# Optimization experiments

Hardware: AMD Instinct MI355X
Metric: run time of the kernel (lower is better)

Reference implementation:

```python
import jax, jax.numpy as jnp
import numpy as np

D_MODEL = 1024
D_STATE = 64
HEADDIM = 64
D_INNER = 2 * D_MODEL          # expand=2 -> 2048
NHEADS = D_INNER // HEADDIM    # 32
D_IN_PROJ = 2 * D_INNER + 2 * D_STATE + NHEADS  # 4256 (ngroups=1)
CHANNELS = D_INNER + 2 * D_STATE                # 2176
KSIZE = 4
LN_EPS = 1e-5


def setup_inputs() -> dict:
    key = jax.random.key(0)
    ks = jax.random.split(key, 8)
    B, L = 2, 2048
    u = jax.random.normal(ks[0], (B, L, D_MODEL), jnp.float32)
    W_in1 = jax.random.normal(ks[1], (D_IN_PROJ, D_MODEL), jnp.float32) * 0.02
    A_log = jnp.log(jax.random.uniform(ks[2], (NHEADS,), jnp.float32, 1.0, 16.0))
    conv_w = jax.random.normal(ks[3], (CHANNELS, CHANNELS, KSIZE), jnp.float32) / np.sqrt(CHANNELS * KSIZE)
    conv_b = jax.random.normal(ks[4], (CHANNELS,), jnp.float32) * 0.01
    prelu_a = jnp.array(0.25, jnp.float32)
    W_in2 = jax.random.normal(ks[5], (D_INNER, D_MODEL), jnp.float32) * 0.02
    W_in3 = jax.random.normal(ks[6], (D_MODEL, D_INNER), jnp.float32) * 0.02
    ln_g = jnp.ones((D_INNER,), jnp.float32)
    ln_b = jnp.zeros((D_INNER,), jnp.float32)
    return {"u": u, "W_in1": W_in1, "A_log": A_log, "conv_w": conv_w, "conv_b": conv_b,
            "prelu_a": prelu_a, "W_in2": W_in2, "W_in3": W_in3, "ln_g": ln_g, "ln_b": ln_b}


def _segsum(x):
    # x: (..., T) -> (..., T, T), lower-triangular segment sums, -inf above diag
    T = x.shape[-1]
    cs = jnp.cumsum(x, axis=-1)
    seg = cs[..., :, None] - cs[..., None, :]
    mask = jnp.tril(jnp.ones((T, T), bool))
    return jnp.where(mask, seg, -jnp.inf)


def _ssd(X, A, B, C, block_len):
    # X:(b,L,h,p)  A:(b,L,h)  B,C:(b,L,n)  (ngroups=1, group axis squeezed)
    b, Lseq, h, p = X.shape
    c = Lseq // block_len
    X = X.reshape(b, c, block_len, h, p)
    A = A.reshape(b, c, block_len, h).transpose(0, 3, 1, 2)      # (b,h,c,l)
    B = B.reshape(b, c, block_len, -1)                            # (b,c,l,n)
    C = C.reshape(b, c, block_len, -1)
    A_cumsum = jnp.cumsum(A, axis=-1)                             # (b,h,c,l)
    Lmat = jnp.exp(_segsum(A))                                    # (b,h,c,l,l)
    Y_diag = jnp.einsum('bcln,bcsn,bhcls,bcshp->bclhp', C, B, Lmat, X)
    decay_states = jnp.exp(A_cumsum[..., -1:] - A_cumsum)         # (b,h,c,l)
    states = jnp.einsum('bcln,bhcl,bclhp->bchpn', B, decay_states, X)
    init = jnp.zeros_like(states[:, :1])
    states = jnp.concatenate([init, states], axis=1)              # (b,c+1,h,p,n)
    A_last = jnp.pad(A_cumsum[..., -1], ((0, 0), (0, 0), (1, 0)))
    decay_chunk = jnp.exp(_segsum(A_last))                        # (b,h,c+1,c+1)
    new_states = jnp.einsum('bhzc,bchpn->bzhpn', decay_chunk, states)
    states_off, final_state = new_states[:, :-1], new_states[:, -1]
    state_decay_out = jnp.exp(A_cumsum)
    Y_off = jnp.einsum('bcln,bchpn,bhcl->bclhp', C, states_off, state_decay_out)
    Y = (Y_diag + Y_off).reshape(b, Lseq, h, p)
    return Y, final_state


def reference(u, W_in1, A_log, conv_w, conv_b, prelu_a, W_in2, W_in3, ln_g, ln_b):
    Bsz, L, _ = u.shape
    zxbcdt = u @ W_in1.T                                          # (B,L,4256); d_nonssm=0
    A = -jnp.exp(A_log)
    z = zxbcdt[..., :D_INNER]                                     # split but unused (as in source)
    xBC = zxbcdt[..., D_INNER:D_INNER + CHANNELS]
    dt = zxbcdt[..., D_INNER + CHANNELS:]
    dt_safe = jnp.where(dt <= 20.0, dt, 0.0)
    dt = jnp.where(dt <= 20.0, jnp.log1p(jnp.exp(dt_safe)), dt)   # softplus w/ overflow guard
    A_t = dt * A[None, None, :]                                   # (B,L,H)
    # causal conv (left-pad k-1) + PReLU
    xt = xBC.transpose(0, 2, 1)                                   # (B,C,L)
    conv = jax.lax.conv_general_dilated(xt, conv_w, (1,), [(KSIZE - 1, 0)],
                                        dimension_numbers=('NCH', 'OIH', 'NCH'))
    conv = conv + conv_b[None, :, None]
    conv = jnp.maximum(conv, 0) + prelu_a * jnp.minimum(conv, 0)
    xBC_conv = conv.transpose(0, 2, 1)                            # (B,L,C)
    x = xBC_conv[..., :D_INNER].reshape(Bsz, L, NHEADS, HEADDIM)
    Bmat = xBC_conv[..., D_INNER:D_INNER + D_STATE]
    Cmat = xBC_conv[..., D_INNER + D_STATE:]
    Y, _ = _ssd(x, A_t, Bmat, Cmat, L // 4)
    out = Y.reshape(Bsz, L, D_INNER)
    u2 = jax.nn.gelu(u @ W_in2.T, approximate=False)
    h = u2 * out
    mu = jnp.mean(h, axis=-1, keepdims=True)
    var = jnp.mean((h - mu) ** 2, axis=-1, keepdims=True)
    hn = (h - mu) / jnp.sqrt(var + LN_EPS) * ln_g + ln_b
    return hn @ W_in3.T
```

## Files before the change

kernel.cpp:

```cpp
#include <hip/hip_runtime.h>
#include <stdint.h>

typedef unsigned short u16;
typedef _Float16 f16x8 __attribute__((ext_vector_type(8)));
typedef float f32x4 __attribute__((ext_vector_type(4)));

#define AS1C const __attribute__((address_space(1))) void*
#define AS3P __attribute__((address_space(3))) void*

#define DM 1024
#define DI 2048
#define CHN 2176
#define ROWS 4096
#define PADR_U 2051

__device__ __forceinline__ float h2f(u16 v) {
    union { u16 u; _Float16 h; } x; x.u = v; return (float)x.h;
}
__device__ __forceinline__ u16 f2h(float f) {
    union { _Float16 h; u16 u; } x; x.h = (_Float16)f; return x.u;
}

template<int EPI, int TERMS>
__global__ __launch_bounds__(256) void split_gemm(
    const u16* __restrict__ Ah, const u16* __restrict__ Al,
    const u16* __restrict__ Bh,
    float* __restrict__ Cf, u16* __restrict__ Oh,
    int K, int ldA, int ldB, int ldC)
{
    __shared__ u16 Ash[128 * 64];
    __shared__ u16 Asl[TERMS == 2 ? 128 * 64 : 64];
    __shared__ u16 Bsh[128 * 64];
    const int tid = threadIdx.x;
    const int bm = blockIdx.x * 128;
    const int bn = blockIdx.y * 128;
    const int lane = tid & 63;
    const int w = tid >> 6, wr = w >> 1, wc = w & 1;
    const int lrow = lane & 15;
    const int cb = lane >> 4;
    const int trow = tid >> 3;
    const int tcolS = (((tid & 7) ^ (trow & 7)) << 3);

    f32x4 acc[4][4];
#pragma unroll
    for (int m = 0; m < 4; ++m)
#pragma unroll
        for (int n = 0; n < 4; ++n) acc[m][n] = f32x4{0.f, 0.f, 0.f, 0.f};

    for (int k0 = 0; k0 < K; k0 += 64) {
#pragma unroll
        for (int ch = 0; ch < 4; ++ch) {
            int r = bm + ch * 32 + trow;
            long aoff = (long)r * ldA + k0 + tcolS;
            __builtin_amdgcn_global_load_lds((AS1C)(Ah + aoff), (AS3P)(&Ash[ch * 2048 + tid * 8]), 16, 0, 0);
            if constexpr (TERMS == 2)
                __builtin_amdgcn_global_load_lds((AS1C)(Al + aoff), (AS3P)(&Asl[ch * 2048 + tid * 8]), 16, 0, 0);
            int rr = bn + ch * 32 + trow;
            long boff = (long)rr * ldB + k0 + tcolS;
            __builtin_amdgcn_global_load_lds((AS1C)(Bh + boff), (AS3P)(&Bsh[ch * 2048 + tid * 8]), 16, 0, 0);
        }
        __syncthreads();
#pragma unroll
        for (int kk = 0; kk < 64; kk += 32) {
            const int swz = ((((kk >> 3) + cb) ^ (lrow & 7)) << 3);
            f16x8 ah[4], al[4], bh[4];
#pragma unroll
            for (int m = 0; m < 4; ++m) {
                int o = (wr * 64 + m * 16 + lrow) * 64 + swz;
                ah[m] = *(const f16x8*)&Ash[o];
                if constexpr (TERMS == 2) al[m] = *(const f16x8*)&Asl[o];
            }
#pragma unroll
            for (int n = 0; n < 4; ++n)
                bh[n] = *(const f16x8*)&Bsh[(wc * 64 + n * 16 + lrow) * 64 + swz];
#pragma unroll
            for (int m = 0; m < 4; ++m)
#pragma unroll
                for (int n = 0; n < 4; ++n) {
                    acc[m][n] = __builtin_amdgcn_mfma_f32_16x16x32_f16(ah[m], bh[n], acc[m][n], 0, 0, 0);
                    if constexpr (TERMS == 2)
                        acc[m][n] = __builtin_amdgcn_mfma_f32_16x16x32_f16(al[m], bh[n], acc[m][n], 0, 0, 0);
                }
        }
        __syncthreads();
    }

#pragma unroll
    for (int m = 0; m < 4; ++m) {
#pragma unroll
        for (int n = 0; n < 4; ++n) {
            int col = bn + wc * 64 + n * 16 + lrow;
            int rbase = bm + wr * 64 + m * 16 + ((lane >> 4) << 2);
#pragma unroll
            for (int j = 0; j < 4; ++j) {
                int r = rbase + j;
                float v = acc[m][n][j];
                if (EPI == 0) {
                    Cf[(long)r * ldC + col] = v;
                } else {
                    int kc = r / CHN;
                    int o = r - kc * CHN;
                    Oh[(long)o * 4096 + kc * 1024 + col] = f2h(v);
                }
            }
        }
    }
}

__global__ __launch_bounds__(256) void conv_g2(
    const u16* __restrict__ up, const u16* __restrict__ Wbig, const u16* __restrict__ W2,
    float* __restrict__ Xf, float* __restrict__ Bm, float* __restrict__ Cm,
    float* __restrict__ u2raw,
    const float* __restrict__ bias, const float* __restrict__ prelu)
{
    __shared__ u16 Ash[128 * 64];
    __shared__ u16 Bsh[128 * 64];
    const int tid = threadIdx.x;
    const bool isconv = blockIdx.y < 17;
    const u16* __restrict__ Bmat = isconv ? Wbig : W2;
    const int K = isconv ? 4096 : 1024;
    const int ldB = K;
    const int aoffR = isconv ? 0 : 3;
    const int bm = blockIdx.x * 128;
    const int bn = (isconv ? blockIdx.y : blockIdx.y - 17) * 128;
    const int lane = tid & 63;
    const int w = tid >> 6, wr = w >> 1, wc = w & 1;
    const int lrow = lane & 15;
    const int cb = lane >> 4;
    const int trow = tid >> 3;
    const int tcolS = (((tid & 7) ^ (trow & 7)) << 3);

    f32x4 acc[4][4];
#pragma unroll
    for (int m = 0; m < 4; ++m)
#pragma unroll
        for (int n = 0; n < 4; ++n) acc[m][n] = f32x4{0.f, 0.f, 0.f, 0.f};

    for (int k0 = 0; k0 < K; k0 += 64) {
        const int kc = k0 >> 10;
        const int i0 = k0 & 1023;
#pragma unroll
        for (int ch = 0; ch < 4; ++ch) {
            int r = bm + ch * 32 + trow;
            long srow = (long)(r >> 11) * PADR_U + (r & 2047) + kc + aoffR;
            long aoff = srow * 1024 + i0 + tcolS;
            __builtin_amdgcn_global_load_lds((AS1C)(up + aoff), (AS3P)(&Ash[ch * 2048 + tid * 8]), 16, 0, 0);
            int rr = bn + ch * 32 + trow;
            long boff = (long)rr * ldB + k0 + tcolS;
            __builtin_amdgcn_global_load_lds((AS1C)(Bmat + boff), (AS3P)(&Bsh[ch * 2048 + tid * 8]), 16, 0, 0);
        }
        __syncthreads();
#pragma unroll
        for (int kk = 0; kk < 64; kk += 32) {
            const int swz = ((((kk >> 3) + cb) ^ (lrow & 7)) << 3);
            f16x8 a[4], b[4];
#pragma unroll
            for (int m = 0; m < 4; ++m)
                a[m] = *(const f16x8*)&Ash[(wr * 64 + m * 16 + lrow) * 64 + swz];
#pragma unroll
            for (int n = 0; n < 4; ++n)
                b[n] = *(const f16x8*)&Bsh[(wc * 64 + n * 16 + lrow) * 64 + swz];
#pragma unroll
            for (int m = 0; m < 4; ++m)
#pragma unroll
                for (int n = 0; n < 4; ++n)
                    acc[m][n] = __builtin_amdgcn_mfma_f32_16x16x32_f16(a[m], b[n], acc[m][n], 0, 0, 0);
        }
        __syncthreads();
    }

    const float pa = isconv ? *prelu : 0.f;
#pragma unroll
    for (int m = 0; m < 4; ++m) {
#pragma unroll
        for (int n = 0; n < 4; ++n) {
            int col = bn + wc * 64 + n * 16 + lrow;
            int rbase = bm + wr * 64 + m * 16 + ((lane >> 4) << 2);
            float bv = isconv ? bias[col] : 0.f;
#pragma unroll
            for (int j = 0; j < 4; ++j) {
                int r = rbase + j;
                float v = acc[m][n][j];
                if (isconv) {
                    v += bv;
                    v = v > 0.f ? v : pa * v;
                    if (col < DI) Xf[(long)r * DI + col] = v;
                    else if (col < DI + 64) Bm[r * 64 + (col - DI)] = v;
                    else Cm[r * 64 + (col - DI - 64)] = v;
                } else {
                    u2raw[(long)r * 2048 + col] = v;
                }
            }
        }
    }
}

__global__ void conv_w_h(const float* __restrict__ w, u16* __restrict__ ch_) {
    int idx = blockIdx.x * 256 + threadIdx.x;
    if (idx < CHN * CHN) {
        int o = idx / CHN, i = idx - o * CHN;
        f32x4 v = *(const f32x4*)&w[(long)idx * 4];
#pragma unroll
        for (int kc = 0; kc < 4; ++kc)
            ch_[(long)(kc * CHN + o) * CHN + i] = f2h(v[kc]);
    }
}

__global__ __launch_bounds__(256) void w1x_t(
    const float* __restrict__ W1, u16* __restrict__ th)
{
    __shared__ float tile[32][33];
    int i0 = blockIdx.x * 32, d0 = blockIdx.y * 32;
    int ti = threadIdx.x & 31, tj = threadIdx.x >> 5;
#pragma unroll
    for (int rr = 0; rr < 32; rr += 8)
        tile[tj + rr][ti] = W1[(long)(2048 + i0 + tj + rr) * 1024 + d0 + ti];
    __syncthreads();
#pragma unroll
    for (int rr = 0; rr < 32; rr += 8)
        th[(long)(d0 + tj + rr) * CHN + i0 + ti] = f2h(tile[ti][tj + rr]);
}

__global__ void u_pad_f16(const float* __restrict__ u, u16* __restrict__ ph) {
    int idx = blockIdx.x * 256 + threadIdx.x;
    if (idx >= 2 * PADR_U * 256) return;
    int row = idx >> 8, c4 = (idx & 255) << 2;
    int b = row >= PADR_U ? 1 : 0;
    int lr = row - b * PADR_U;
    ushort4 h = {0, 0, 0, 0};
    if (lr >= 3) {
        f32x4 v = *(const f32x4*)&u[((long)(b * 2048 + lr - 3)) * 1024 + c4];
        h.x = f2h(v[0]); h.y = f2h(v[1]); h.z = f2h(v[2]); h.w = f2h(v[3]);
    }
    *(ushort4*)&ph[(long)idx * 4] = h;
}

__global__ void cast_f16(const float* __restrict__ in, u16* __restrict__ oh, int n4) {
    int idx = blockIdx.x * 256 + threadIdx.x;
    if (idx < n4) {
        f32x4 v = *(const f32x4*)&in[(long)idx * 4];
        ushort4 h;
        h.x = f2h(v[0]); h.y = f2h(v[1]); h.z = f2h(v[2]); h.w = f2h(v[3]);
        *(ushort4*)&oh[(long)idx * 4] = h;
    }
}

__global__ __launch_bounds__(256) void dt_kernel(
    const float* __restrict__ u, const float* __restrict__ W1,
    const float* __restrict__ A_log, float* __restrict__ A_t)
{
    __shared__ float us[8][1024];
    int r0 = blockIdx.x * 8;
    int tid = threadIdx.x;
#pragma unroll
    for (int rep = 0; rep < 8; ++rep) {
        int idx = rep * 256 + tid;
        int i = idx >> 8, kx = (idx & 255) << 2;
        *(f32x4*)&us[i][kx] = *(const f32x4*)&u[(long)(r0 + i) * 1024 + kx];
    }
    __syncthreads();
    int row = tid >> 5;
    int hh = tid & 31;
    const float* wrow = W1 + (long)(4224 + hh) * 1024;
    f32x4 a4 = {0.f, 0.f, 0.f, 0.f};
#pragma unroll 4
    for (int k = 0; k < 1024; k += 4) {
        f32x4 a = *(const f32x4*)&us[row][k];
        f32x4 b = *(const f32x4*)&wrow[k];
        a4 += a * b;
    }
    float dt = a4[0] + a4[1] + a4[2] + a4[3];
    if (dt <= 20.f) dt = log1pf(__expf(dt));
    float At = dt * (-__expf(A_log[hh]));
    int r = r0 + row;
    int b = r >> 11, l = r & 2047;
    A_t[((long)(b * 32 + hh)) * 2048 + l] = At;
}

__global__ __launch_bounds__(64) void csum_chunk(float* A_t, float* __restrict__ Atot)
{
    int bid = blockIdx.x;
    int lane = threadIdx.x;
    float* p = A_t + (long)bid * 128;
    float v0 = p[lane * 2], v1 = p[lane * 2 + 1];
    float s = v0 + v1;
    float t = s;
#pragma unroll
    for (int d = 1; d < 64; d <<= 1) {
        float o = __shfl_up(t, d);
        if (lane >= d) t += o;
    }
    float excl = t - s;
    p[lane * 2] = excl + v0;
    p[lane * 2 + 1] = excl + s;
    if (lane == 63) Atot[bid] = t;
}

__global__ __launch_bounds__(256) void g_chunk(
    const float* __restrict__ Cm, const float* __restrict__ Bm, float* __restrict__ G)
{
    __shared__ float CsT[128 * 33];
    __shared__ float BsT[128 * 33];
    const int bid = blockIdx.x;
    const int b = bid >> 4, c = bid & 15;
    const long rowbase = (long)b * 2048 + c * 128;
    const int tid = threadIdx.x;
    const int li = tid & 15, si = tid >> 4;
    const int l0 = li * 8, s0 = si * 8;
    float acc[8][8];
#pragma unroll
    for (int i = 0; i < 8; ++i)
#pragma unroll
        for (int j = 0; j < 8; ++j) acc[i][j] = 0.f;

    for (int kt = 0; kt < 2; ++kt) {
        __syncthreads();
#pragma unroll
        for (int t = 0; t < 16; ++t) {
            int idx = t * 256 + tid;
            int row = idx >> 5, k = idx & 31;
            CsT[row * 33 + k] = Cm[(rowbase + row) * 64 + kt * 32 + k];
            BsT[row * 33 + k] = Bm[(rowbase + row) * 64 + kt * 32 + k];
        }
        __syncthreads();
        for (int k = 0; k < 32; ++k) {
            float cv[8], bv[8];
#pragma unroll
            for (int i = 0; i < 8; ++i) cv[i] = CsT[(l0 + i) * 33 + k];
#pragma unroll
            for (int j = 0; j < 8; ++j) bv[j] = BsT[(s0 + j) * 33 + k];
#pragma unroll
            for (int i = 0; i < 8; ++i)
#pragma unroll
                for (int j = 0; j < 8; ++j) acc[i][j] += cv[i] * bv[j];
        }
    }
    float* gz = G + (long)bid * 16384;
#pragma unroll
    for (int i = 0; i < 8; ++i) {
        f32x4 o0 = {acc[i][0], acc[i][1], acc[i][2], acc[i][3]};
        f32x4 o1 = {acc[i][4], acc[i][5], acc[i][6], acc[i][7]};
        *(f32x4*)&gz[(l0 + i) * 128 + s0] = o0;
        *(f32x4*)&gz[(l0 + i) * 128 + s0 + 4] = o1;
    }
}

__global__ __launch_bounds__(256) void ssd_diag_states(
    float* XY, const float* __restrict__ Bm, const float* __restrict__ G,
    const float* __restrict__ cs, const float* __restrict__ Atot, float* __restrict__ Sc)
{
    __shared__ float Xs[128 * 64];
    __shared__ float Gb[32 * 132];
    __shared__ float csL[128];
    __shared__ float dsL[128];
    const int bid = blockIdx.x;
    const int bh = bid >> 4, c = bid & 15;
    const int b = bh >> 5, h = bh & 31;
    const long rowbase = (long)b * 2048 + c * 128;
    const float* gz = G + (long)(b * 16 + c) * 16384;
    const float atot = Atot[bid];
    const int tid = threadIdx.x;

    if (tid < 128) csL[tid] = cs[(long)bh * 2048 + c * 128 + tid];
#pragma unroll
    for (int t = 0; t < 8; ++t) {
        int idx = t * 256 + tid;
        int row = idx >> 4, c4 = (idx & 15) << 2;
        *(f32x4*)&Xs[row * 64 + c4] = *(const f32x4*)&XY[(rowbase + row) * 2048 + h * 64 + c4];
    }
    __syncthreads();
    if (tid < 128) dsL[tid] = __expf(atot - csL[tid]);

    const int lg = tid & 31, pg = tid >> 5;
    const int l0 = lg * 4, p0 = pg * 8;
    float cl[4];
#pragma unroll
    for (int i = 0; i < 4; ++i) cl[i] = csL[l0 + i];
    float acc1[4][8];
#pragma unroll
    for (int i = 0; i < 4; ++i)
#pragma unroll
        for (int j = 0; j < 8; ++j) acc1[i][j] = 0.f;

    for (int st = 0; st < 4; ++st) {
        __syncthreads();
#pragma unroll
        for (int t = 0; t < 16; ++t) {
            int idx = t * 256 + tid;
            int l = idx >> 5, sq = idx & 31;
            Gb[sq * 132 + l] = gz[l * 128 + st * 32 + sq];
        }
        __syncthreads();
        for (int sq = 0; sq < 32; ++sq) {
            int s = st * 32 + sq;
            float css = csL[s];
            f32x4 x0 = *(const f32x4*)&Xs[s * 64 + p0];
            f32x4 x1 = *(const f32x4*)&Xs[s * 64 + p0 + 4];
#pragma unroll
            for (int i = 0; i < 4; ++i) {
                int l = l0 + i;
                float P = (s <= l) ? Gb[sq * 132 + l] * __expf(cl[i] - css) : 0.f;
                acc1[i][0] += P * x0[0]; acc1[i][1] += P * x0[1];
                acc1[i][2] += P * x0[2]; acc1[i][3] += P * x0[3];
                acc1[i][4] += P * x1[0]; acc1[i][5] += P * x1[1];
                acc1[i][6] += P * x1[2]; acc1[i][7] += P * x1[3];
            }
        }
    }

    const int pq = tid & 15, nq = tid >> 4;
    const int pp0 = pq * 4, nn0 = nq * 4;
    float acc2[4][4];
#pragma unroll
    for (int i = 0; i < 4; ++i)
#pragma unroll
        for (int j = 0; j < 4; ++j) acc2[i][j] = 0.f;
    for (int half = 0; half < 2; ++half) {
        __syncthreads();
#pragma unroll
        for (int t = 0; t < 4; ++t) {
            int idx = t * 256 + tid;
            int srow = idx >> 4, c4 = (idx & 15) << 2;
            *(f32x4*)&Gb[srow * 64 + c4] = *(const f32x4*)&Bm[(rowbase + half * 64 + srow) * 64 + c4];
        }
        __syncthreads();
        for (int ss = 0; ss < 64; ++ss) {
            int s = half * 64 + ss;
            float d = dsL[s];
            f32x4 xv = *(const f32x4*)&Xs[s * 64 + pp0];
            f32x4 bv = *(const f32x4*)&Gb[ss * 64 + nn0];
            float xd[4];
#pragma unroll
            for (int i = 0; i < 4; ++i) xd[i] = xv[i] * d;
#pragma unroll
            for (int i = 0; i < 4; ++i)
#pragma unroll
                for (int j = 0; j < 4; ++j) acc2[i][j] += xd[i] * bv[j];
        }
    }
    long scb = (long)bid * 4096;
#pragma unroll
    for (int i = 0; i < 4; ++i) {
        f32x4 o = {acc2[i][0], acc2[i][1], acc2[i][2], acc2[i][3]};
        *(f32x4*)&Sc[scb + (pp0 + i) * 64 + nn0] = o;
    }
#pragma unroll
    for (int i = 0; i < 4; ++i) {
        f32x4 y0 = {acc1[i][0], acc1[i][1], acc1[i][2], acc1[i][3]};
        f32x4 y1 = {acc1[i][4], acc1[i][5], acc1[i][6], acc1[i][7]};
        long yo = (rowbase + l0 + i) * 2048 + h * 64 + p0;
        *(f32x4*)&XY[yo] = y0;
        *(f32x4*)&XY[yo + 4] = y1;
    }
}

__global__ __launch_bounds__(256) void ssd_combine(float* Sc, const float* __restrict__ Atot)
{
    int bh = blockIdx.x >> 2;
    int q = blockIdx.x & 3;
    int tid = threadIdx.x;
    float run[4];
#pragma unroll
    for (int t = 0; t < 4; ++t) run[t] = 0.f;
    for (int c = 0; c < 16; ++c) {
        float e = __expf(Atot[bh * 16 + c]);
        long base = (long)(bh * 16 + c) * 4096 + q * 1024;
#pragma unroll
        for (int t = 0; t < 4; ++t) {
            long idx = base + t * 256 + tid;
            float tmp = Sc[idx];
            Sc[idx] = run[t];
            run[t] = e * run[t] + tmp;
        }
    }
}

__global__ __launch_bounds__(256) void ssd_yoff(
    const float* __restrict__ Cm, const float* __restrict__ Sin,
    const float* __restrict__ cs, float* XY)
{
    __shared__ float Cs[128 * 66];
    __shared__ float St[64 * 68];
    __shared__ float csL[128];
    const int bid = blockIdx.x;
    const int bh = bid >> 4, c = bid & 15;
    const int b = bh >> 5, h = bh & 31;
    const long rowbase = (long)b * 2048 + c * 128;
    const int tid = threadIdx.x;

    if (tid < 128) csL[tid] = cs[(long)bh * 2048 + c * 128 + tid];
#pragma unroll
    for (int t = 0; t < 32; ++t) {
        int idx = t * 256 + tid;
        int row = idx >> 6, n = idx & 63;
        Cs[row * 66 + n] = Cm[(rowbase + row) * 64 + n];
    }
#pragma unroll
    for (int t = 0; t < 16; ++t) {
        int idx = t * 256 + tid;
        int p = idx >> 6, n = idx & 63;
        St[n * 68 + p] = Sin[(long)bid * 4096 + p * 64 + n];
    }
    __syncthreads();

    const int lg = tid & 31, pg = tid >> 5;
    const int l0 = lg * 4, p0 = pg * 8;
    float el[4];
#pragma unroll
    for (int i = 0; i < 4; ++i) el[i] = __expf(csL[l0 + i]);
    float acc[4][8];
#pragma unroll
    for (int i = 0; i < 4; ++i)
#pragma unroll
        for (int j = 0; j < 8; ++j) acc[i][j] = 0.f;

    for (int n = 0; n < 64; ++n) {
        float cv[4];
#pragma unroll
        for (int i = 0; i < 4; ++i) cv[i] = Cs[(l0 + i) * 66 + n];
        f32x4 s0 = *(const f32x4*)&St[n * 68 + p0];
        f32x4 s1 = *(const f32x4*)&St[n * 68 + p0 + 4];
#pragma unroll
        for (int i = 0; i < 4; ++i) {
            acc[i][0] += cv[i] * s0[0]; acc[i][1] += cv[i] * s0[1];
            acc[i][2] += cv[i] * s0[2]; acc[i][3] += cv[i] * s0[3];
            acc[i][4] += cv[i] * s1[0]; acc[i][5] += cv[i] * s1[1];
            acc[i][6] += cv[i] * s1[2]; acc[i][7] += cv[i] * s1[3];
        }
    }
#pragma unroll
    for (int i = 0; i < 4; ++i) {
        long yo = (rowbase + l0 + i) * 2048 + h * 64 + p0;
        f32x4 y0 = *(const f32x4*)&XY[yo];
        f32x4 y1 = *(const f32x4*)&XY[yo + 4];
        y0[0] += el[i] * acc[i][0]; y0[1] += el[i] * acc[i][1];
        y0[2] += el[i] * acc[i][2]; y0[3] += el[i] * acc[i][3];
        y1[0] += el[i] * acc[i][4]; y1[1] += el[i] * acc[i][5];
        y1[2] += el[i] * acc[i][6]; y1[3] += el[i] * acc[i][7];
        *(f32x4*)&XY[yo] = y0;
        *(f32x4*)&XY[yo + 4] = y1;
    }
}

__global__ __launch_bounds__(256) void ln_kernel(
    const float* __restrict__ u2raw, const float* __restrict__ Y,
    const float* __restrict__ lng, const float* __restrict__ lnb,
    u16* __restrict__ hh)
{
    __shared__ float hbuf[2048];
    __shared__ float rs[4], rs2[4];
    int r = blockIdx.x;
    int tid = threadIdx.x;
    float s = 0.f, s2 = 0.f;
    for (int j = tid; j < 2048; j += 256) {
        float x = u2raw[(long)r * 2048 + j];
        float g = 0.5f * x * (1.f + erff(x * 0.70710678118654752f));
        float hv = g * Y[(long)r * 2048 + j];
        hbuf[j] = hv;
        s += hv;
        s2 += hv * hv;
    }
    for (int d = 32; d > 0; d >>= 1) {
        s += __shfl_down(s, d);
        s2 += __shfl_down(s2, d);
    }
    if ((tid & 63) == 0) { rs[tid >> 6] = s; rs2[tid >> 6] = s2; }
    __syncthreads();
    float tot = rs[0] + rs[1] + rs[2] + rs[3];
    float tot2 = rs2[0] + rs2[1] + rs2[2] + rs2[3];
    float mu = tot * (1.f / 2048.f);
    float var = tot2 * (1.f / 2048.f) - mu * mu;
    float inv = rsqrtf(var + 1e-5f);
    for (int j = tid; j < 2048; j += 256) {
        float v = (hbuf[j] - mu) * inv * lng[j] + lnb[j];
        hh[(long)r * 2048 + j] = f2h(v);
    }
}

extern "C" void kernel_launch(void* const* d_in, const int* in_sizes, int n_in,
                              void* d_out, int out_size, void* d_ws, size_t ws_size,
                              hipStream_t stream) {
    const float* u = (const float*)d_in[0];
    const float* W1 = (const float*)d_in[1];
    const float* A_log = (const float*)d_in[2];
    const float* convw = (const float*)d_in[3];
    const float* convb = (const float*)d_in[4];
    const float* prelu = (const float*)d_in[5];
    const float* W2 = (const float*)d_in[6];
    const float* W3 = (const float*)d_in[7];
    const float* lng = (const float*)d_in[8];
    const float* lnb = (const float*)d_in[9];
    float* out = (float*)d_out;

    char* base = (char*)d_ws;
    size_t off = 0;
    auto nxt = [&](size_t bytes) -> char* {
        char* r = base + off;
        off = (off + bytes + 255) & ~(size_t)255;
        return r;
    };
    u16* cw_h = (u16*)nxt((size_t)4 * CHN * CHN * 2);
    float* u2raw = (float*)cw_h;
    u16* hn_h = (u16*)nxt((size_t)ROWS * DI * 2);
    u16* up_h = (u16*)nxt((size_t)2 * PADR_U * 1024 * 2);
    u16* w1t_h = (u16*)nxt((size_t)1024 * CHN * 2);
    float* Gbuf = (float*)w1t_h;
    u16* wbig_h = (u16*)nxt((size_t)CHN * 4096 * 2);
    u16* w2_h = (u16*)nxt((size_t)DI * DM * 2);
    u16* w3_h = (u16*)nxt((size_t)DM * DI * 2);
    float* A_t = (float*)nxt((size_t)64 * 2048 * 4);
    float* Atot = (float*)nxt((size_t)64 * 16 * 4);
    float* XY = (float*)nxt((size_t)ROWS * DI * 4);
    float* Bmat = (float*)nxt((size_t)ROWS * 64 * 4);
    float* Cmat = (float*)nxt((size_t)ROWS * 64 * 4);
    float* Sc = (float*)nxt((size_t)64 * 16 * 4096 * 4);

    conv_w_h<<<(CHN * CHN + 255) / 256, 256, 0, stream>>>(convw, cw_h);
    w1x_t<<<dim3(68, 32), 256, 0, stream>>>(W1, w1t_h);
    u_pad_f16<<<(2 * PADR_U * 256 + 255) / 256, 256, 0, stream>>>(u, up_h);
    cast_f16<<<DI * DM / 1024, 256, 0, stream>>>(W2, w2_h, DI * DM / 4);
    cast_f16<<<DM * DI / 1024, 256, 0, stream>>>(W3, w3_h, DM * DI / 4);
    dt_kernel<<<512, 256, 0, stream>>>(u, W1, A_log, A_t);
    csum_chunk<<<1024, 64, 0, stream>>>(A_t, Atot);

    split_gemm<3, 1><<<dim3(68, 8), 256, 0, stream>>>(
        cw_h, nullptr, w1t_h, nullptr, wbig_h, 2176, 2176, 2176, 0);

    conv_g2<<<dim3(32, 33), 256, 0, stream>>>(
        up_h, wbig_h, w2_h, XY, Bmat, Cmat, u2raw, convb, prelu);

    g_chunk<<<32, 256, 0, stream>>>(Cmat, Bmat, Gbuf);
    ssd_diag_states<<<1024, 256, 0, stream>>>(XY, Bmat, Gbuf, A_t, Atot, Sc);
    ssd_combine<<<256, 256, 0, stream>>>(Sc, Atot);
    ssd_yoff<<<1024, 256, 0, stream>>>(Cmat, Sc, A_t, XY);

    ln_kernel<<<4096, 256, 0, stream>>>(u2raw, XY, lng, lnb, hn_h);

    split_gemm<0, 1><<<dim3(32, 8), 256, 0, stream>>>(
        hn_h, nullptr, w3_h, out, nullptr, 2048, 2048, 2048, 1024);
}
```

Before: 532.8 us.

## Regroup launches: fuse weight-fold GEMM with u·W2 GEMM, merge small prep kernels

Moves the u·W2 GEMM out of the conv kernel and into a new combined launch alongside the conv-weight folding GEMM, interleaving their tiles so the independent work shares one grid. It also fuses the u padding/cast into the dt kernel, merges the two weight casts into one launch, and merges the chunk cumsum with the G computation. The goal is to cut launch count and fill the GPU better on previously undersized grids. u2raw gets its own buffer, which adds workspace, and the conv GEMM now runs as a separate smaller grid.

Result: slower. 582.0 us (+9.2%).

```diff
diff --git a/kernel.cpp b/kernel.cpp
--- a/kernel.cpp
+++ b/kernel.cpp
@@ -21,15 +21,13 @@
     union { _Float16 h; u16 u; } x; x.h = (_Float16)f; return x.u;
 }
 
-template<int EPI, int TERMS>
+template<int EPI>
 __global__ __launch_bounds__(256) void split_gemm(
-    const u16* __restrict__ Ah, const u16* __restrict__ Al,
-    const u16* __restrict__ Bh,
-    float* __restrict__ Cf, u16* __restrict__ Oh,
+    const u16* __restrict__ Ah, const u16* __restrict__ Bh,
+    float* __restrict__ Cf,
     int K, int ldA, int ldB, int ldC)
 {
     __shared__ u16 Ash[128 * 64];
-    __shared__ u16 Asl[TERMS == 2 ? 128 * 64 : 64];
     __shared__ u16 Bsh[128 * 64];
     const int tid = threadIdx.x;
     const int bm = blockIdx.x * 128;
@@ -53,8 +51,6 @@
             int r = bm + ch * 32 + trow;
             long aoff = (long)r * ldA + k0 + tcolS;
             __builtin_amdgcn_global_load_lds((AS1C)(Ah + aoff), (AS3P)(&Ash[ch * 2048 + tid * 8]), 16, 0, 0);
-            if constexpr (TERMS == 2)
-                __builtin_amdgcn_global_load_lds((AS1C)(Al + aoff), (AS3P)(&Asl[ch * 2048 + tid * 8]), 16, 0, 0);
             int rr = bn + ch * 32 + trow;
             long boff = (long)rr * ldB + k0 + tcolS;
             __builtin_amdgcn_global_load_lds((AS1C)(Bh + boff), (AS3P)(&Bsh[ch * 2048 + tid * 8]), 16, 0, 0);
@@ -63,24 +59,18 @@
 #pragma unroll
         for (int kk = 0; kk < 64; kk += 32) {
             const int swz = ((((kk >> 3) + cb) ^ (lrow & 7)) << 3);
-            f16x8 ah[4], al[4], bh[4];
-#pragma unroll
-            for (int m = 0; m < 4; ++m) {
-                int o = (wr * 64 + m * 16 + lrow) * 64 + swz;
-                ah[m] = *(const f16x8*)&Ash[o];
-                if constexpr (TERMS == 2) al[m] = *(const f16x8*)&Asl[o];
-            }
+            f16x8 a[4], b[4];
+#pragma unroll
+            for (int m = 0; m < 4; ++m)
+                a[m] = *(const f16x8*)&Ash[(wr * 64 + m * 16 + lrow) * 64 + swz];
 #pragma unroll
             for (int n = 0; n < 4; ++n)
-                bh[n] = *(const f16x8*)&Bsh[(wc * 64 + n * 16 + lrow) * 64 + swz];
+                b[n] = *(const f16x8*)&Bsh[(wc * 64 + n * 16 + lrow) * 64 + swz];
 #pragma unroll
             for (int m = 0; m < 4; ++m)
 #pragma unroll
-                for (int n = 0; n < 4; ++n) {
-                    acc[m][n] = __builtin_amdgcn_mfma_f32_16x16x32_f16(ah[m], bh[n], acc[m][n], 0, 0, 0);
-                    if constexpr (TERMS == 2)
-                        acc[m][n] = __builtin_amdgcn_mfma_f32_16x16x32_f16(al[m], bh[n], acc[m][n], 0, 0, 0);
-                }
+                for (int n = 0; n < 4; ++n)
+                    acc[m][n] = __builtin_amdgcn_mfma_f32_16x16x32_f16(a[m], b[n], acc[m][n], 0, 0, 0);
         }
         __syncthreads();
     }
@@ -94,35 +84,30 @@
 #pragma unroll
             for (int j = 0; j < 4; ++j) {
                 int r = rbase + j;
-                float v = acc[m][n][j];
-                if (EPI == 0) {
-                    Cf[(long)r * ldC + col] = v;
-                } else {
-                    int kc = r / CHN;
-                    int o = r - kc * CHN;
-                    Oh[(long)o * 4096 + kc * 1024 + col] = f2h(v);
-                }
+                Cf[(long)r * ldC + col] = acc[m][n][j];
             }
         }
     }
 }
 
-__global__ __launch_bounds__(256) void conv_g2(
-    const u16* __restrict__ up, const u16* __restrict__ Wbig, const u16* __restrict__ W2,
-    float* __restrict__ Xf, float* __restrict__ Bm, float* __restrict__ Cm,
-    float* __restrict__ u2raw,
-    const float* __restrict__ bias, const float* __restrict__ prelu)
+__global__ __launch_bounds__(256) void wg2_kernel(
+    const u16* __restrict__ cw, const u16* __restrict__ w1t,
+    const u16* __restrict__ up, const u16* __restrict__ w2,
+    u16* __restrict__ wbig, float* __restrict__ u2raw)
 {
     __shared__ u16 Ash[128 * 64];
     __shared__ u16 Bsh[128 * 64];
     const int tid = threadIdx.x;
-    const bool isconv = blockIdx.y < 17;
-    const u16* __restrict__ Bmat = isconv ? Wbig : W2;
-    const int K = isconv ? 4096 : 1024;
+    int id = blockIdx.x;
+    bool isW; int wid;
+    if (id < 1024) { isW = (id & 1) == 0; wid = id >> 1; }
+    else { isW = true; wid = 512 + (id - 1024); }
+    const u16* __restrict__ A = isW ? cw : up;
+    const u16* __restrict__ B = isW ? w1t : w2;
+    const int bm = (isW ? (wid % 68) : (wid & 31)) * 128;
+    const int bn = (isW ? (wid / 68) : (wid >> 5)) * 128;
+    const int K = isW ? 2176 : 1024;
     const int ldB = K;
-    const int aoffR = isconv ? 0 : 3;
-    const int bm = blockIdx.x * 128;
-    const int bn = (isconv ? blockIdx.y : blockIdx.y - 17) * 128;
     const int lane = tid & 63;
     const int w = tid >> 6, wr = w >> 1, wc = w & 1;
     const int lrow = lane & 15;
@@ -137,17 +122,98 @@
         for (int n = 0; n < 4; ++n) acc[m][n] = f32x4{0.f, 0.f, 0.f, 0.f};
 
     for (int k0 = 0; k0 < K; k0 += 64) {
+#pragma unroll
+        for (int ch = 0; ch < 4; ++ch) {
+            int r = bm + ch * 32 + trow;
+            long aoff;
+            if (isW) {
+                aoff = (long)r * 2176 + k0 + tcolS;
+            } else {
+                long srow = (long)(r >> 11) * PADR_U + (r & 2047) + 3;
+                aoff = srow * 1024 + k0 + tcolS;
+            }
+            __builtin_amdgcn_global_load_lds((AS1C)(A + aoff), (AS3P)(&Ash[ch * 2048 + tid * 8]), 16, 0, 0);
+            int rr = bn + ch * 32 + trow;
+            long boff = (long)rr * ldB + k0 + tcolS;
+            __builtin_amdgcn_global_load_lds((AS1C)(B + boff), (AS3P)(&Bsh[ch * 2048 + tid * 8]), 16, 0, 0);
+        }
+        __syncthreads();
+#pragma unroll
+        for (int kk = 0; kk < 64; kk += 32) {
+            const int swz = ((((kk >> 3) + cb) ^ (lrow & 7)) << 3);
+            f16x8 a[4], b[4];
+#pragma unroll
+            for (int m = 0; m < 4; ++m)
+                a[m] = *(const f16x8*)&Ash[(wr * 64 + m * 16 + lrow) * 64 + swz];
+#pragma unroll
+            for (int n = 0; n < 4; ++n)
+                b[n] = *(const f16x8*)&Bsh[(wc * 64 + n * 16 + lrow) * 64 + swz];
+#pragma unroll
+            for (int m = 0; m < 4; ++m)
+#pragma unroll
+                for (int n = 0; n < 4; ++n)
+                    acc[m][n] = __builtin_amdgcn_mfma_f32_16x16x32_f16(a[m], b[n], acc[m][n], 0, 0, 0);
+        }
+        __syncthreads();
+    }
+
+#pragma unroll
+    for (int m = 0; m < 4; ++m) {
+#pragma unroll
+        for (int n = 0; n < 4; ++n) {
+            int col = bn + wc * 64 + n * 16 + lrow;
+            int rbase = bm + wr * 64 + m * 16 + ((lane >> 4) << 2);
+#pragma unroll
+            for (int j = 0; j < 4; ++j) {
+                int r = rbase + j;
+                float v = acc[m][n][j];
+                if (isW) {
+                    int kc = r / CHN;
+                    int o = r - kc * CHN;
+                    wbig[(long)o * 4096 + kc * 1024 + col] = f2h(v);
+                } else {
+                    u2raw[(long)r * 2048 + col] = v;
+                }
+            }
+        }
+    }
+}
+
+__global__ __launch_bounds__(256) void conv_k(
+    const u16* __restrict__ up, const u16* __restrict__ Wbig,
+    float* __restrict__ Xf, float* __restrict__ Bm, float* __restrict__ Cm,
+    const float* __restrict__ bias, const float* __restrict__ prelu)
+{
+    __shared__ u16 Ash[128 * 64];
+    __shared__ u16 Bsh[128 * 64];
+    const int tid = threadIdx.x;
+    const int bm = blockIdx.x * 128;
+    const int bn = blockIdx.y * 128;
+    const int lane = tid & 63;
+    const int w = tid >> 6, wr = w >> 1, wc = w & 1;
+    const int lrow = lane & 15;
+    const int cb = lane >> 4;
+    const int trow = tid >> 3;
+    const int tcolS = (((tid & 7) ^ (trow & 7)) << 3);
+
+    f32x4 acc[4][4];
+#pragma unroll
+    for (int m = 0; m < 4; ++m)
+#pragma unroll
+        for (int n = 0; n < 4; ++n) acc[m][n] = f32x4{0.f, 0.f, 0.f, 0.f};
+
+    for (int k0 = 0; k0 < 4096; k0 += 64) {
         const int kc = k0 >> 10;
         const int i0 = k0 & 1023;
 #pragma unroll
         for (int ch = 0; ch < 4; ++ch) {
             int r = bm + ch * 32 + trow;
-            long srow = (long)(r >> 11) * PADR_U + (r & 2047) + kc + aoffR;
+            long srow = (long)(r >> 11) * PADR_U + (r & 2047) + kc;
             long aoff = srow * 1024 + i0 + tcolS;
             __builtin_amdgcn_global_load_lds((AS1C)(up + aoff), (AS3P)(&Ash[ch * 2048 + tid * 8]), 16, 0, 0);
             int rr = bn + ch * 32 + trow;
-            long boff = (long)rr * ldB + k0 + tcolS;
-            __builtin_amdgcn_global_load_lds((AS1C)(Bmat + boff), (AS3P)(&Bsh[ch * 2048 + tid * 8]), 16, 0, 0);
+            long boff = (long)rr * 4096 + k0 + tcolS;
+            __builtin_amdgcn_global_load_lds((AS1C)(Wbig + boff), (AS3P)(&Bsh[ch * 2048 + tid * 8]), 16, 0, 0);
         }
         __syncthreads();
 #pragma unroll
@@ -169,27 +235,22 @@
         __syncthreads();
     }
 
-    const float pa = isconv ? *prelu : 0.f;
+    const float pa = *prelu;
 #pragma unroll
     for (int m = 0; m < 4; ++m) {
 #pragma unroll
         for (int n = 0; n < 4; ++n) {
             int col = bn + wc * 64 + n * 16 + lrow;
             int rbase = bm + wr * 64 + m * 16 + ((lane >> 4) << 2);
-            float bv = isconv ? bias[col] : 0.f;
+            float bv = bias[col];
 #pragma unroll
             for (int j = 0; j < 4; ++j) {
                 int r = rbase + j;
-                float v = acc[m][n][j];
-                if (isconv) {
-                    v += bv;
-                    v = v > 0.f ? v : pa * v;
-                    if (col < DI) Xf[(long)r * DI + col] = v;
-                    else if (col < DI + 64) Bm[r * 64 + (col - DI)] = v;
-                    else Cm[r * 64 + (col - DI - 64)] = v;
-                } else {
-                    u2raw[(long)r * 2048 + col] = v;
-                }
+                float v = acc[m][n][j] + bv;
+                v = v > 0.f ? v : pa * v;
+                if (col < DI) Xf[(long)r * DI + col] = v;
+                else if (col < DI + 64) Bm[r * 64 + (col - DI)] = v;
+                else Cm[r * 64 + (col - DI - 64)] = v;
             }
         }
     }
@@ -221,33 +282,9 @@
         th[(long)(d0 + tj + rr) * CHN + i0 + ti] = f2h(tile[ti][tj + rr]);
 }
 
-__global__ void u_pad_f16(const float* __restrict__ u, u16* __restrict__ ph) {
-    int idx = blockIdx.x * 256 + threadIdx.x;
-    if (idx >= 2 * PADR_U * 256) return;
-    int row = idx >> 8, c4 = (idx & 255) << 2;
-    int b = row >= PADR_U ? 1 : 0;
-    int lr = row - b * PADR_U;
-    ushort4 h = {0, 0, 0, 0};
-    if (lr >= 3) {
-        f32x4 v = *(const f32x4*)&u[((long)(b * 2048 + lr - 3)) * 1024 + c4];
-        h.x = f2h(v[0]); h.y = f2h(v[1]); h.z = f2h(v[2]); h.w = f2h(v[3]);
-    }
-    *(ushort4*)&ph[(long)idx * 4] = h;
-}
-
-__global__ void cast_f16(const float* __restrict__ in, u16* __restrict__ oh, int n4) {
-    int idx = blockIdx.x * 256 + threadIdx.x;
-    if (idx < n4) {
-        f32x4 v = *(const f32x4*)&in[(long)idx * 4];
-        ushort4 h;
-        h.x = f2h(v[0]); h.y = f2h(v[1]); h.z = f2h(v[2]); h.w = f2h(v[3]);
-        *(ushort4*)&oh[(long)idx * 4] = h;
-    }
-}
-
-__global__ __launch_bounds__(256) void dt_kernel(
+__global__ __launch_bounds__(256) void u_pad_dt(
     const float* __restrict__ u, const float* __restrict__ W1,
-    const float* __restrict__ A_log, float* __restrict__ A_t)
+    const float* __restrict__ A_log, u16* __restrict__ ph, float* __restrict__ A_t)
 {
     __shared__ float us[8][1024];
     int r0 = blockIdx.x * 8;
@@ -259,6 +296,17 @@
         *(f32x4*)&us[i][kx] = *(const f32x4*)&u[(long)(r0 + i) * 1024 + kx];
     }
     __syncthreads();
+#pragma unroll
+    for (int rep = 0; rep < 8; ++rep) {
+        int idx = rep * 256 + tid;
+        int i = idx >> 8, kx = (idx & 255) << 2;
+        int r = r0 + i;
+        long prow = (long)(r >> 11) * PADR_U + 3 + (r & 2047);
+        f32x4 v = *(const f32x4*)&us[i][kx];
+        ushort4 h;
+        h.x = f2h(v[0]); h.y = f2h(v[1]); h.z = f2h(v[2]); h.w = f2h(v[3]);
+        *(ushort4*)&ph[prow * 1024 + kx] = h;
+    }
     int row = tid >> 5;
     int hh = tid & 31;
     const float* wrow = W1 + (long)(4224 + hh) * 1024;
@@ -277,31 +325,54 @@
     A_t[((long)(b * 32 + hh)) * 2048 + l] = At;
 }
 
-__global__ __launch_bounds__(64) void csum_chunk(float* A_t, float* __restrict__ Atot)
-{
-    int bid = blockIdx.x;
-    int lane = threadIdx.x;
-    float* p = A_t + (long)bid * 128;
-    float v0 = p[lane * 2], v1 = p[lane * 2 + 1];
-    float s = v0 + v1;
-    float t = s;
-#pragma unroll
-    for (int d = 1; d < 64; d <<= 1) {
-        float o = __shfl_up(t, d);
-        if (lane >= d) t += o;
-    }
-    float excl = t - s;
-    p[lane * 2] = excl + v0;
-    p[lane * 2 + 1] = excl + s;
-    if (lane == 63) Atot[bid] = t;
-}
-
-__global__ __launch_bounds__(256) void g_chunk(
+__global__ void zero_pad_u(u16* __restrict__ ph) {
+    int t = blockIdx.x * 256 + threadIdx.x;
+    if (t < 3 * 1024) {
+        ph[t] = 0;
+        ph[(long)PADR_U * 1024 + t] = 0;
+    }
+}
+
+__global__ void cast2_f16(const float* __restrict__ a, u16* __restrict__ oa,
+                          const float* __restrict__ b, u16* __restrict__ ob, int n4) {
+    int idx = blockIdx.x * 256 + threadIdx.x;
+    const float* src;
+    u16* dst;
+    if (idx < n4) { src = a; dst = oa; }
+    else if (idx < 2 * n4) { idx -= n4; src = b; dst = ob; }
+    else return;
+    f32x4 v = *(const f32x4*)&src[(long)idx * 4];
+    ushort4 h;
+    h.x = f2h(v[0]); h.y = f2h(v[1]); h.z = f2h(v[2]); h.w = f2h(v[3]);
+    *(ushort4*)&dst[(long)idx * 4] = h;
+}
+
+__global__ __launch_bounds__(256) void csum_g(
+    float* A_t, float* __restrict__ Atot,
     const float* __restrict__ Cm, const float* __restrict__ Bm, float* __restrict__ G)
 {
+    if (blockIdx.x < 1024) {
+        if (threadIdx.x >= 64) return;
+        int bid = blockIdx.x;
+        int lane = threadIdx.x;
+        float* p = A_t + (long)bid * 128;
+        float v0 = p[lane * 2], v1 = p[lane * 2 + 1];
+        float s = v0 + v1;
+        float t = s;
+#pragma unroll
+        for (int d = 1; d < 64; d <<= 1) {
+            float o = __shfl_up(t, d);
+            if (lane >= d) t += o;
+        }
+        float excl = t - s;
+        p[lane * 2] = excl + v0;
+        p[lane * 2 + 1] = excl + s;
+        if (lane == 63) Atot[bid] = t;
+        return;
+    }
     __shared__ float CsT[128 * 33];
     __shared__ float BsT[128 * 33];
-    const int bid = blockIdx.x;
+    const int bid = blockIdx.x - 1024;
     const int b = bid >> 4, c = bid & 15;
     const long rowbase = (long)b * 2048 + c * 128;
     const int tid = threadIdx.x;
@@ -600,8 +671,8 @@
         return r;
     };
     u16* cw_h = (u16*)nxt((size_t)4 * CHN * CHN * 2);
-    float* u2raw = (float*)cw_h;
-    u16* hn_h = (u16*)nxt((size_t)ROWS * DI * 2);
+    u16* hn_h = cw_h;
+    float* u2raw = (float*)nxt((size_t)ROWS * DI * 4);
     u16* up_h = (u16*)nxt((size_t)2 * PADR_U * 1024 * 2);
     u16* w1t_h = (u16*)nxt((size_t)1024 * CHN * 2);
     float* Gbuf = (float*)w1t_h;
@@ -617,25 +688,22 @@
 
     conv_w_h<<<(CHN * CHN + 255) / 256, 256, 0, stream>>>(convw, cw_h);
     w1x_t<<<dim3(68, 32), 256, 0, stream>>>(W1, w1t_h);
-    u_pad_f16<<<(2 * PADR_U * 256 + 255) / 256, 256, 0, stream>>>(u, up_h);
-    cast_f16<<<DI * DM / 1024, 256, 0, stream>>>(W2, w2_h, DI * DM / 4);
-    cast_f16<<<DM * DI / 1024, 256, 0, stream>>>(W3, w3_h, DM * DI / 4);
-    dt_kernel<<<512, 256, 0, stream>>>(u, W1, A_log, A_t);
-    csum_chunk<<<1024, 64, 0, stream>>>(A_t, Atot);
-
-    split_gemm<3, 1><<<dim3(68, 8), 256, 0, stream>>>(
-        cw_h, nullptr, w1t_h, nullptr, wbig_h, 2176, 2176, 2176, 0);
-
-    conv_g2<<<dim3(32, 33), 256, 0, stream>>>(
-        up_h, wbig_h, w2_h, XY, Bmat, Cmat, u2raw, convb, prelu);
-
-    g_chunk<<<32, 256, 0, stream>>>(Cmat, Bmat, Gbuf);
+    u_pad_dt<<<512, 256, 0, stream>>>(u, W1, A_log, up_h, A_t);
+    zero_pad_u<<<12, 256, 0, stream>>>(up_h);
+    cast2_f16<<<(2 * DI * DM / 4 + 255) / 256, 256, 0, stream>>>(
+        W2, w2_h, W3, w3_h, DI * DM / 4);
+
+    wg2_kernel<<<1056, 256, 0, stream>>>(cw_h, w1t_h, up_h, w2_h, wbig_h, u2raw);
+
+    conv_k<<<dim3(32, 17), 256, 0, stream>>>(up_h, wbig_h, XY, Bmat, Cmat, convb, prelu);
+
+    csum_g<<<1056, 256, 0, stream>>>(A_t, Atot, Cmat, Bmat, Gbuf);
     ssd_diag_states<<<1024, 256, 0, stream>>>(XY, Bmat, Gbuf, A_t, Atot, Sc);
     ssd_combine<<<256, 256, 0, stream>>>(Sc, Atot);
     ssd_yoff<<<1024, 256, 0, stream>>>(Cmat, Sc, A_t, XY);
 
     ln_kernel<<<4096, 256, 0, stream>>>(u2raw, XY, lng, lnb, hn_h);
 
-    split_gemm<0, 1><<<dim3(32, 8), 256, 0, stream>>>(
-        hn_h, nullptr, w3_h, out, nullptr, 2048, 2048, 2048, 1024);
-}
+    split_gemm<0><<<dim3(32, 8), 256, 0, stream>>>(
+        hn_h, w3_h, out, 2048, 2048, 2048, 1024);
+}
```
